# Optimization experiments

Measured on AMD Instinct MI355X. Metric: run time of the kernel, lower is better.

Reference implementation:

```python
import jax, jax.numpy as jnp
import numpy as np

N_NODES = 50000
N_EDGES = 800000
IN_DIM = 128
HID_DIM = 128
OUT_DIM = 64


def setup_inputs() -> dict:
    key = jax.random.key(0)
    ks = jax.random.split(key, 6)
    x = jax.random.normal(ks[0], (N_NODES, IN_DIM), dtype=jnp.float32)
    row = jax.random.randint(ks[1], (N_EDGES,), 0, N_NODES, dtype=jnp.int32)
    col = jax.random.randint(ks[2], (N_EDGES,), 0, N_NODES, dtype=jnp.int32)
    vals = jax.random.uniform(ks[3], (N_EDGES,), dtype=jnp.float32)
    # Xavier-uniform init as in nn.init.xavier_uniform_
    lim1 = float(np.sqrt(6.0 / (IN_DIM + HID_DIM)))
    lim2 = float(np.sqrt(6.0 / (HID_DIM + OUT_DIM)))
    W1 = jax.random.uniform(ks[4], (IN_DIM, HID_DIM), minval=-lim1, maxval=lim1, dtype=jnp.float32)
    W2 = jax.random.uniform(ks[5], (HID_DIM, OUT_DIM), minval=-lim2, maxval=lim2, dtype=jnp.float32)
    return {"x": x, "row": row, "col": col, "vals": vals, "W1": W1, "W2": W2}


def _spmm(row, col, vals, x):
    # out[i] = sum_{e: row[e]==i} vals[e] * x[col[e]]   (sparse adj @ x)
    msgs = vals[:, None] * x[col]  # [E, D] gathered edge messages
    return jax.ops.segment_sum(msgs, row, num_segments=N_NODES)


def reference(x, row, col, vals, W1, W2):
    # GCN layer 1: adj.mm(x) -> linear -> relu  (dropout = identity in eval)
    h = jax.nn.relu(_spmm(row, col, vals, x) @ W1)
    # GCN layer 2: adj.mm(h) -> linear (no activation)
    out = _spmm(row, col, vals, h) @ W2
    return out
```

## Files before the change

kernel.cpp:

```cpp
#include <hip/hip_runtime.h>
#include <stdint.h>

#define N_NODES 50000
#define N_EDGES 800000
#define IN_DIM 128
#define HID_DIM 128
#define OUT_DIM 64

#define ELL_CAP 64
#define XCD_GROUPS 8
#define ROWS_PER_XCD (N_NODES / XCD_GROUPS)
#define SCAT_BLOCKS_PER_XCD 128
#define SCAT_BLOCKS (SCAT_BLOCKS_PER_XCD * XCD_GROUPS)
#define GEMM1_BLOCKS 392

typedef short bf16x8 __attribute__((ext_vector_type(8)));
typedef float f32x4  __attribute__((ext_vector_type(4)));

__device__ __forceinline__ uint32_t pack_bf16x2(float a, float b) {
    uint32_t ba = __float_as_uint(a), bb = __float_as_uint(b);
    ba = (ba + 0x7fffu + ((ba >> 16) & 1u)) >> 16;
    bb = (bb + 0x7fffu + ((bb >> 16) & 1u)) & 0xffff0000u;
    return ba | bb;
}

__device__ __forceinline__ unsigned short f2bf(float f) {
    uint32_t u = __float_as_uint(f);
    return (unsigned short)((u + 0x7fffu + ((u >> 16) & 1u)) >> 16);
}

__device__ __forceinline__ uint8_t f2fp8(float f) {
    uint32_t u = __float_as_uint(f);
    uint32_t s = (u >> 24) & 0x80u;
    uint32_t au = u & 0x7fffffffu;
    uint32_t r = au + 0x7FFFFu + ((au >> 20) & 1u);
    int e = (int)((r >> 23) & 0xffu) - 120;
    uint32_t m = (r >> 20) & 7u;
    uint32_t out;
    if (e <= 0) out = 0u;
    else if (e >= 16) out = 0x7Eu;
    else out = ((uint32_t)e << 3) | m;
    return (uint8_t)(s | out);
}

__device__ __forceinline__ uint32_t pack_edge(int col, float v) {
    uint32_t fb = __float_as_uint(v);
    fb = (fb + 0x7fffu + ((fb >> 16) & 1u)) & 0xffff0000u;
    return fb | (uint32_t)col;
}


__global__ __launch_bounds__(256) void zero_convert(int* __restrict__ counts,
                                                    const float* __restrict__ W1,
                                                    const float* __restrict__ W2,
                                                    unsigned short* __restrict__ wt1,
                                                    unsigned short* __restrict__ wt2) {
    int i = blockIdx.x * 256 + threadIdx.x;
    if (i < N_NODES) counts[i] = 0;
    int j = i - N_NODES;
    if (j >= 0 && j < 128 * 128) {
        int n = j >> 7, k = j & 127;
        wt1[j] = f2bf(W1[k * 128 + n]);
    }
    int l = j - 128 * 128;
    if (l >= 0 && l < 64 * 128) {
        int n = l >> 7, k = l & 127;
        wt2[l] = f2bf(W2[k * 64 + n]);
    }
}


__global__ __launch_bounds__(256) void fused_scatter_gemm1(const int* __restrict__ row,
                                                           const int* __restrict__ col,
                                                           const float* __restrict__ vals,
                                                           int* __restrict__ counts,
                                                           uint32_t* __restrict__ ell,
                                                           const float* __restrict__ x,
                                                           const unsigned short* __restrict__ wt1,
                                                           uint8_t* __restrict__ t1f8) {
    if (blockIdx.x < SCAT_BLOCKS) {
        const int xcd = blockIdx.x & (XCD_GROUPS - 1);
        const int blk = blockIdx.x >> 3;
        const int rlo = xcd * ROWS_PER_XCD;
        int e = blk * 256 + threadIdx.x;
        const int stride = SCAT_BLOCKS_PER_XCD * 256;
        for (; e < N_EDGES; e += stride) {
            int r = row[e];
            if ((unsigned)(r - rlo) < (unsigned)ROWS_PER_XCD) {
                int p = atomicAdd(&counts[r], 1);
                if (p < ELL_CAP)
                    ell[((size_t)r << 6) + p] = pack_edge(col[e], vals[e]);
            }
        }
        return;
    }

    const int g  = blockIdx.x - SCAT_BLOCKS;
    const int bx = g % 196;
    const int n0 = (g / 196) * 64;
    const int tid = threadIdx.x;
    const int wid = tid >> 6, lane = tid & 63;
    const int l15 = lane & 15, lk = lane >> 4;

    bf16x8 bfrag[4][4];
#pragma unroll
    for (int t = 0; t < 4; ++t) {
        const unsigned short* wp = wt1 + (size_t)(n0 + t * 16 + l15) * 128 + lk * 8;
#pragma unroll
        for (int s = 0; s < 4; ++s)
            bfrag[t][s] = *reinterpret_cast<const bf16x8*>(wp + s * 32);
    }

    for (int mt = bx * 4 + wid; mt < 3125; mt += 784) {
        const int arow = mt * 16 + l15;
        bf16x8 afrag[4];
        const float* ap = x + (size_t)arow * 128 + lk * 8;
#pragma unroll
        for (int s = 0; s < 4; ++s) {
            float4 p0 = *reinterpret_cast<const float4*>(ap + s * 32);
            float4 p1 = *reinterpret_cast<const float4*>(ap + s * 32 + 4);
            bf16x8 f;
            f[0] = (short)f2bf(p0.x); f[1] = (short)f2bf(p0.y);
            f[2] = (short)f2bf(p0.z); f[3] = (short)f2bf(p0.w);
            f[4] = (short)f2bf(p1.x); f[5] = (short)f2bf(p1.y);
            f[6] = (short)f2bf(p1.z); f[7] = (short)f2bf(p1.w);
            afrag[s] = f;
        }

        f32x4 acc[4] = {{0.f,0.f,0.f,0.f},{0.f,0.f,0.f,0.f},{0.f,0.f,0.f,0.f},{0.f,0.f,0.f,0.f}};
#pragma unroll
        for (int s = 0; s < 4; ++s)
#pragma unroll
            for (int t = 0; t < 4; ++t)
                acc[t] = __builtin_amdgcn_mfma_f32_16x16x32_bf16(afrag[s], bfrag[t][s], acc[t], 0, 0, 0);

#pragma unroll
        for (int t = 0; t < 4; ++t)
#pragma unroll
            for (int q = 0; q < 4; ++q) {
                int r = mt * 16 + lk * 4 + q;
                t1f8[(size_t)r * 128 + n0 + t * 16 + l15] = f2fp8(acc[t][q]);
            }
    }
}


__global__ __launch_bounds__(256) void gemm_mfma2(const uint32_t* __restrict__ Apk,
                                                  const unsigned short* __restrict__ Wt,
                                                  unsigned short* __restrict__ outb) {
    const int tid = threadIdx.x;
    const int wid = tid >> 6, lane = tid & 63;
    const int l15 = lane & 15, lk = lane >> 4;

    bf16x8 bfrag[4][4];
#pragma unroll
    for (int t = 0; t < 4; ++t) {
        const unsigned short* wp = Wt + (size_t)(t * 16 + l15) * 128 + lk * 8;
#pragma unroll
        for (int s = 0; s < 4; ++s)
            bfrag[t][s] = *reinterpret_cast<const bf16x8*>(wp + s * 32);
    }

    for (int mt = blockIdx.x * 4 + wid; mt < 3125; mt += 784) {
        const int arow = mt * 16 + l15;
        bf16x8 afrag[4];
        const uint32_t* ap = Apk + (size_t)arow * 64 + lk * 4;
#pragma unroll
        for (int s = 0; s < 4; ++s)
            afrag[s] = *reinterpret_cast<const bf16x8*>(ap + s * 16);

        f32x4 acc[4] = {{0.f,0.f,0.f,0.f},{0.f,0.f,0.f,0.f},{0.f,0.f,0.f,0.f},{0.f,0.f,0.f,0.f}};
#pragma unroll
        for (int s = 0; s < 4; ++s)
#pragma unroll
            for (int t = 0; t < 4; ++t)
                acc[t] = __builtin_amdgcn_mfma_f32_16x16x32_bf16(afrag[s], bfrag[t][s], acc[t], 0, 0, 0);

#pragma unroll
        for (int t = 0; t < 4; ++t)
#pragma unroll
            for (int q = 0; q < 4; ++q) {
                int r = mt * 16 + lk * 4 + q;
                outb[(size_t)r * 64 + t * 16 + l15] = f2bf(acc[t][q]);
            }
    }
}


template<bool RELU>
__global__ __launch_bounds__(256) void spmm_fp8_128(const int* __restrict__ counts,
                                                    const uint32_t* __restrict__ ell,
                                                    const uint8_t* __restrict__ x8,
                                                    uint32_t* __restrict__ outp) {
    __shared__ float lut[256];
    {
        int b = threadIdx.x;
        uint32_t ee = (b >> 3) & 15u, mm = b & 7u;
        float f = (ee == 0) ? ldexpf((float)mm, -9) : ldexpf((float)(8 + mm), (int)ee - 10);
        lut[b] = (b & 0x80) ? -f : f;
    }
    __syncthreads();

    const int wid = threadIdx.x >> 6;
    const int lane = threadIdx.x & 63;
    const int r = blockIdx.x * 4 + wid;
    if (r >= N_NODES) return;
    const int start = r << 6;
    int cnt = counts[r]; if (cnt > ELL_CAP) cnt = ELL_CAP;
    const int end = start + cnt;
    const uint8_t* xb = x8 + lane * 2;

    float alo[4] = {0.f, 0.f, 0.f, 0.f};
    float ahi[4] = {0.f, 0.f, 0.f, 0.f};
    int e = start;
    for (; e + 7 < end; e += 8) {
        uint32_t c0 = ell[e],     c1 = ell[e + 1], c2 = ell[e + 2], c3 = ell[e + 3];
        uint32_t c4 = ell[e + 4], c5 = ell[e + 5], c6 = ell[e + 6], c7 = ell[e + 7];
        unsigned short u0 = *reinterpret_cast<const unsigned short*>(xb + (size_t)(c0 & 0xffffu) * 128);
        unsigned short u1 = *reinterpret_cast<const unsigned short*>(xb + (size_t)(c1 & 0xffffu) * 128);
        unsigned short u2 = *reinterpret_cast<const unsigned short*>(xb + (size_t)(c2 & 0xffffu) * 128);
        unsigned short u3 = *reinterpret_cast<const unsigned short*>(xb + (size_t)(c3 & 0xffffu) * 128);
        unsigned short u4 = *reinterpret_cast<const unsigned short*>(xb + (size_t)(c4 & 0xffffu) * 128);
        unsigned short u5 = *reinterpret_cast<const unsigned short*>(xb + (size_t)(c5 & 0xffffu) * 128);
        unsigned short u6 = *reinterpret_cast<const unsigned short*>(xb + (size_t)(c6 & 0xffffu) * 128);
        unsigned short u7 = *reinterpret_cast<const unsigned short*>(xb + (size_t)(c7 & 0xffffu) * 128);
        float v0 = __uint_as_float(c0 & 0xffff0000u), v1 = __uint_as_float(c1 & 0xffff0000u);
        float v2 = __uint_as_float(c2 & 0xffff0000u), v3 = __uint_as_float(c3 & 0xffff0000u);
        float v4 = __uint_as_float(c4 & 0xffff0000u), v5 = __uint_as_float(c5 & 0xffff0000u);
        float v6 = __uint_as_float(c6 & 0xffff0000u), v7 = __uint_as_float(c7 & 0xffff0000u);
        alo[0] = fmaf(v0, lut[u0 & 0xff], alo[0]); ahi[0] = fmaf(v0, lut[u0 >> 8], ahi[0]);
        alo[1] = fmaf(v1, lut[u1 & 0xff], alo[1]); ahi[1] = fmaf(v1, lut[u1 >> 8], ahi[1]);
        alo[2] = fmaf(v2, lut[u2 & 0xff], alo[2]); ahi[2] = fmaf(v2, lut[u2 >> 8], ahi[2]);
        alo[3] = fmaf(v3, lut[u3 & 0xff], alo[3]); ahi[3] = fmaf(v3, lut[u3 >> 8], ahi[3]);
        alo[0] = fmaf(v4, lut[u4 & 0xff], alo[0]); ahi[0] = fmaf(v4, lut[u4 >> 8], ahi[0]);
        alo[1] = fmaf(v5, lut[u5 & 0xff], alo[1]); ahi[1] = fmaf(v5, lut[u5 >> 8], ahi[1]);
        alo[2] = fmaf(v6, lut[u6 & 0xff], alo[2]); ahi[2] = fmaf(v6, lut[u6 >> 8], ahi[2]);
        alo[3] = fmaf(v7, lut[u7 & 0xff], alo[3]); ahi[3] = fmaf(v7, lut[u7 >> 8], ahi[3]);
    }
    if (e + 3 < end) {
        uint32_t c0 = ell[e], c1 = ell[e + 1], c2 = ell[e + 2], c3 = ell[e + 3];
        unsigned short u0 = *reinterpret_cast<const unsigned short*>(xb + (size_t)(c0 & 0xffffu) * 128);
        unsigned short u1 = *reinterpret_cast<const unsigned short*>(xb + (size_t)(c1 & 0xffffu) * 128);
        unsigned short u2 = *reinterpret_cast<const unsigned short*>(xb + (size_t)(c2 & 0xffffu) * 128);
        unsigned short u3 = *reinterpret_cast<const unsigned short*>(xb + (size_t)(c3 & 0xffffu) * 128);
        float v0 = __uint_as_float(c0 & 0xffff0000u), v1 = __uint_as_float(c1 & 0xffff0000u);
        float v2 = __uint_as_float(c2 & 0xffff0000u), v3 = __uint_as_float(c3 & 0xffff0000u);
        alo[0] = fmaf(v0, lut[u0 & 0xff], alo[0]); ahi[0] = fmaf(v0, lut[u0 >> 8], ahi[0]);
        alo[1] = fmaf(v1, lut[u1 & 0xff], alo[1]); ahi[1] = fmaf(v1, lut[u1 >> 8], ahi[1]);
        alo[2] = fmaf(v2, lut[u2 & 0xff], alo[2]); ahi[2] = fmaf(v2, lut[u2 >> 8], ahi[2]);
        alo[3] = fmaf(v3, lut[u3 & 0xff], alo[3]); ahi[3] = fmaf(v3, lut[u3 >> 8], ahi[3]);
        e += 4;
    }
    for (; e < end; ++e) {
        uint32_t c0 = ell[e];
        float v0 = __uint_as_float(c0 & 0xffff0000u);
        unsigned short u0 = *reinterpret_cast<const unsigned short*>(xb + (size_t)(c0 & 0xffffu) * 128);
        alo[0] = fmaf(v0, lut[u0 & 0xff], alo[0]); ahi[0] = fmaf(v0, lut[u0 >> 8], ahi[0]);
    }
    float rlo = (alo[0] + alo[1]) + (alo[2] + alo[3]);
    float rhi = (ahi[0] + ahi[1]) + (ahi[2] + ahi[3]);
    if (RELU) { rlo = fmaxf(rlo, 0.f); rhi = fmaxf(rhi, 0.f); }
    outp[(size_t)r * 64 + lane] = pack_bf16x2(rlo, rhi);
}


__global__ __launch_bounds__(256) void spmm_bf16_64(const int* __restrict__ counts,
                                                    const uint32_t* __restrict__ ell,
                                                    const uint32_t* __restrict__ xp,
                                                    float* __restrict__ out) {
    const int wid = threadIdx.x >> 6;
    const int lane = threadIdx.x & 63;
    const int r = blockIdx.x * 4 + wid;
    if (r >= N_NODES) return;
    const int start = r << 6;
    int cnt = counts[r]; if (cnt > ELL_CAP) cnt = ELL_CAP;
    const int end = start + cnt;
    const int j = lane & 31;
    const int half = lane >> 5;
    const uint32_t* xb = xp + j;

    float alo[4] = {0.f, 0.f, 0.f, 0.f};
    float ahi[4] = {0.f, 0.f, 0.f, 0.f};
    int e = start + half;
    for (; e + 6 < end; e += 8) {
        uint32_t c0 = ell[e], c1 = ell[e + 2], c2 = ell[e + 4], c3 = ell[e + 6];
        uint32_t u0 = xb[(size_t)(c0 & 0xffffu) * 32];
        uint32_t u1 = xb[(size_t)(c1 & 0xffffu) * 32];
        uint32_t u2 = xb[(size_t)(c2 & 0xffffu) * 32];
        uint32_t u3 = xb[(size_t)(c3 & 0xffffu) * 32];
        float v0 = __uint_as_float(c0 & 0xffff0000u), v1 = __uint_as_float(c1 & 0xffff0000u);
        float v2 = __uint_as_float(c2 & 0xffff0000u), v3 = __uint_as_float(c3 & 0xffff0000u);
        alo[0] = fmaf(v0, __uint_as_float(u0 << 16), alo[0]);
        ahi[0] = fmaf(v0, __uint_as_float(u0 & 0xffff0000u), ahi[0]);
        alo[1] = fmaf(v1, __uint_as_float(u1 << 16), alo[1]);
        ahi[1] = fmaf(v1, __uint_as_float(u1 & 0xffff0000u), ahi[1]);
        alo[2] = fmaf(v2, __uint_as_float(u2 << 16), alo[2]);
        ahi[2] = fmaf(v2, __uint_as_float(u2 & 0xffff0000u), ahi[2]);
        alo[3] = fmaf(v3, __uint_as_float(u3 << 16), alo[3]);
        ahi[3] = fmaf(v3, __uint_as_float(u3 & 0xffff0000u), ahi[3]);
    }
    for (; e < end; e += 2) {
        uint32_t c0 = ell[e];
        float v = __uint_as_float(c0 & 0xffff0000u);
        uint32_t u = xb[(size_t)(c0 & 0xffffu) * 32];
        alo[0] = fmaf(v, __uint_as_float(u << 16), alo[0]);
        ahi[0] = fmaf(v, __uint_as_float(u & 0xffff0000u), ahi[0]);
    }
    float alo_s = (alo[0] + alo[1]) + (alo[2] + alo[3]);
    float ahi_s = (ahi[0] + ahi[1]) + (ahi[2] + ahi[3]);
    alo_s += __shfl_xor(alo_s, 32);
    ahi_s += __shfl_xor(ahi_s, 32);
    if (half == 0) {
        float2 res = {alo_s, ahi_s};
        *reinterpret_cast<float2*>(out + (size_t)r * 64 + j * 2) = res;
    }
}


extern "C" void kernel_launch(void* const* d_in, const int* in_sizes, int n_in,
                              void* d_out, int out_size, void* d_ws, size_t ws_size,
                              hipStream_t stream) {
    const float* x    = (const float*)d_in[0];
    const int*   row  = (const int*)  d_in[1];
    const int*   col  = (const int*)  d_in[2];
    const float* vals = (const float*)d_in[3];
    const float* W1   = (const float*)d_in[4];
    const float* W2   = (const float*)d_in[5];
    float* out = (float*)d_out;

    char* ws = (char*)d_ws;
    auto align = [](size_t v) { return (v + 255) & ~(size_t)255; };
    int*      counts  = (int*)ws;              ws += align(sizeof(int) * N_NODES);
    uint32_t* ell     = (uint32_t*)ws;         ws += align(sizeof(uint32_t) * N_NODES * ELL_CAP);
    uint8_t*  t1f8    = (uint8_t*)ws;          ws += align(sizeof(uint8_t) * N_NODES * 128);
    uint32_t* hpk     = (uint32_t*)ws;         ws += align(sizeof(uint32_t) * N_NODES * 64);
    uint32_t* tpk     = (uint32_t*)ws;         ws += align(sizeof(uint32_t) * N_NODES * 32);
    unsigned short* wt1 = (unsigned short*)ws; ws += align(sizeof(short) * 128 * 128);
    unsigned short* wt2 = (unsigned short*)ws; ws += align(sizeof(short) * 64 * 128);

    zero_convert<<<(N_NODES + 128 * 128 + 64 * 128 + 255) / 256, 256, 0, stream>>>(counts, W1, W2, wt1, wt2);

    fused_scatter_gemm1<<<SCAT_BLOCKS + GEMM1_BLOCKS, 256, 0, stream>>>(
        row, col, vals, counts, ell, x, wt1, t1f8);

    spmm_fp8_128<true><<<(N_NODES + 3) / 4, 256, 0, stream>>>(counts, ell, t1f8, hpk);

    gemm_mfma2<<<196, 256, 0, stream>>>(hpk, wt2, (unsigned short*)tpk);
    spmm_bf16_64<<<(N_NODES + 3) / 4, 256, 0, stream>>>(counts, ell, tpk, out);
}
```

Before: 133.9 us.

## Split fused scatter/GEMM1 kernel and prepack edges in init kernel

Undoes the fusion of the ELL scatter and the first GEMM into a single launch and splits them into separate scatter_ell and gemm_mfma1 kernels. Edge packing (col plus bf16 value) moves into the init kernel, which now also runs over all edges and writes a packed edge array. The scatter then reads one packed word per edge instead of col and vals on the predicated path. This adds a kernel launch, an extra 3.2MB write and read, and gives up the overlap between scatter and GEMM1.

```diff
diff --git a/kernel.cpp b/kernel.cpp
--- a/kernel.cpp
+++ b/kernel.cpp
@@ -12,7 +12,8 @@
 #define ROWS_PER_XCD (N_NODES / XCD_GROUPS)
 #define SCAT_BLOCKS_PER_XCD 128
 #define SCAT_BLOCKS (SCAT_BLOCKS_PER_XCD * XCD_GROUPS)
-#define GEMM1_BLOCKS 392
+
+#define INIT_BLOCKS 3300
 
 typedef short bf16x8 __attribute__((ext_vector_type(8)));
 typedef float f32x4  __attribute__((ext_vector_type(4)));
@@ -50,11 +51,14 @@
 }
 
 
-__global__ __launch_bounds__(256) void zero_convert(int* __restrict__ counts,
-                                                    const float* __restrict__ W1,
-                                                    const float* __restrict__ W2,
-                                                    unsigned short* __restrict__ wt1,
-                                                    unsigned short* __restrict__ wt2) {
+__global__ __launch_bounds__(256) void init_all(int* __restrict__ counts,
+                                                const float* __restrict__ W1,
+                                                const float* __restrict__ W2,
+                                                unsigned short* __restrict__ wt1,
+                                                unsigned short* __restrict__ wt2,
+                                                const int* __restrict__ col,
+                                                const float* __restrict__ vals,
+                                                uint32_t* __restrict__ epk) {
     int i = blockIdx.x * 256 + threadIdx.x;
     if (i < N_NODES) counts[i] = 0;
     int j = i - N_NODES;
@@ -67,40 +71,37 @@
         int n = l >> 7, k = l & 127;
         wt2[l] = f2bf(W2[k * 64 + n]);
     }
-}
-
-
-__global__ __launch_bounds__(256) void fused_scatter_gemm1(const int* __restrict__ row,
-                                                           const int* __restrict__ col,
-                                                           const float* __restrict__ vals,
-                                                           int* __restrict__ counts,
-                                                           uint32_t* __restrict__ ell,
-                                                           const float* __restrict__ x,
-                                                           const unsigned short* __restrict__ wt1,
-                                                           uint8_t* __restrict__ t1f8) {
-    if (blockIdx.x < SCAT_BLOCKS) {
-        const int xcd = blockIdx.x & (XCD_GROUPS - 1);
-        const int blk = blockIdx.x >> 3;
-        const int rlo = xcd * ROWS_PER_XCD;
-        int e = blk * 256 + threadIdx.x;
-        const int stride = SCAT_BLOCKS_PER_XCD * 256;
-        for (; e < N_EDGES; e += stride) {
-            int r = row[e];
-            if ((unsigned)(r - rlo) < (unsigned)ROWS_PER_XCD) {
-                int p = atomicAdd(&counts[r], 1);
-                if (p < ELL_CAP)
-                    ell[((size_t)r << 6) + p] = pack_edge(col[e], vals[e]);
-            }
+    if (i < N_EDGES) epk[i] = pack_edge(col[i], vals[i]);
+}
+
+
+__global__ __launch_bounds__(256) void scatter_ell(const int* __restrict__ row,
+                                                   const uint32_t* __restrict__ epk,
+                                                   int* __restrict__ counts,
+                                                   uint32_t* __restrict__ ell) {
+    const int xcd = blockIdx.x & (XCD_GROUPS - 1);
+    const int blk = blockIdx.x >> 3;
+    const int rlo = xcd * ROWS_PER_XCD;
+    int e = blk * 256 + threadIdx.x;
+    const int stride = SCAT_BLOCKS_PER_XCD * 256;
+    for (; e < N_EDGES; e += stride) {
+        int r = row[e];
+        if ((unsigned)(r - rlo) < (unsigned)ROWS_PER_XCD) {
+            int p = atomicAdd(&counts[r], 1);
+            if (p < ELL_CAP)
+                ell[((size_t)r << 6) + p] = epk[e];
         }
-        return;
-    }
-
-    const int g  = blockIdx.x - SCAT_BLOCKS;
-    const int bx = g % 196;
-    const int n0 = (g / 196) * 64;
+    }
+}
+
+
+__global__ __launch_bounds__(256) void gemm_mfma1(const float* __restrict__ x,
+                                                  const unsigned short* __restrict__ wt1,
+                                                  uint8_t* __restrict__ t1f8) {
     const int tid = threadIdx.x;
     const int wid = tid >> 6, lane = tid & 63;
     const int l15 = lane & 15, lk = lane >> 4;
+    const int n0 = blockIdx.y * 64;
 
     bf16x8 bfrag[4][4];
 #pragma unroll
@@ -111,7 +112,7 @@
             bfrag[t][s] = *reinterpret_cast<const bf16x8*>(wp + s * 32);
     }
 
-    for (int mt = bx * 4 + wid; mt < 3125; mt += 784) {
+    for (int mt = blockIdx.x * 4 + wid; mt < 3125; mt += 784) {
         const int arow = mt * 16 + l15;
         bf16x8 afrag[4];
         const float* ap = x + (size_t)arow * 128 + lk * 8;
@@ -331,6 +332,7 @@
     char* ws = (char*)d_ws;
     auto align = [](size_t v) { return (v + 255) & ~(size_t)255; };
     int*      counts  = (int*)ws;              ws += align(sizeof(int) * N_NODES);
+    uint32_t* epk     = (uint32_t*)ws;         ws += align(sizeof(uint32_t) * N_EDGES);
     uint32_t* ell     = (uint32_t*)ws;         ws += align(sizeof(uint32_t) * N_NODES * ELL_CAP);
     uint8_t*  t1f8    = (uint8_t*)ws;          ws += align(sizeof(uint8_t) * N_NODES * 128);
     uint32_t* hpk     = (uint32_t*)ws;         ws += align(sizeof(uint32_t) * N_NODES * 64);
@@ -338,11 +340,11 @@
     unsigned short* wt1 = (unsigned short*)ws; ws += align(sizeof(short) * 128 * 128);
     unsigned short* wt2 = (unsigned short*)ws; ws += align(sizeof(short) * 64 * 128);
 
-    zero_convert<<<(N_NODES + 128 * 128 + 64 * 128 + 255) / 256, 256, 0, stream>>>(counts, W1, W2, wt1, wt2);
-
-    fused_scatter_gemm1<<<SCAT_BLOCKS + GEMM1_BLOCKS, 256, 0, stream>>>(
-        row, col, vals, counts, ell, x, wt1, t1f8);
-
+    init_all<<<INIT_BLOCKS, 256, 0, stream>>>(counts, W1, W2, wt1, wt2, col, vals, epk);
+
+    scatter_ell<<<SCAT_BLOCKS, 256, 0, stream>>>(row, epk, counts, ell);
+
+    gemm_mfma1<<<dim3(196, 2), 256, 0, stream>>>(x, wt1, t1f8);
     spmm_fp8_128<true><<<(N_NODES + 3) / 4, 256, 0, stream>>>(counts, ell, t1f8, hpk);
 
     gemm_mfma2<<<196, 256, 0, stream>>>(hpk, wt2, (unsigned short*)tpk);
```

After: 128.2 us. -4.2%, faster.
